# Kernel optimization log

Hardware: AMD Instinct MI355X
Metric: run time of the kernel (lower is better)

The kernel has to match this reference:

```python
import jax, jax.numpy as jnp
import numpy as np

N_EXPERTS = 8
TOPK = 2


def setup_inputs() -> dict:
    key = jax.random.key(0)
    k1, k2, k3, k4 = jax.random.split(key, 4)
    B, T, D, H, E = 2, 2048, 1024, 4096, N_EXPERTS
    s = 1.0 / np.sqrt(D)
    return {
        "x": jax.random.normal(k1, (B, T, D), dtype=jnp.float32),
        "W_gate": jax.random.normal(k2, (E, D), dtype=jnp.float32) * s,
        "W_fc": jax.random.normal(k3, (E, H, D), dtype=jnp.float32) * s,
        "W_proj": jax.random.normal(k4, (E, D, H), dtype=jnp.float32) * (1.0 / np.sqrt(H)),
    }


def reference(x, W_gate, W_fc, W_proj):
    B, T, D = x.shape
    E = W_gate.shape[0]
    N = B * T
    xf = x.reshape(N, D)

    # gating
    gate_logits = xf @ W_gate.T                       # [N, E]
    gate_probs = jax.nn.softmax(gate_logits, axis=-1)
    rw, eidx = jax.lax.top_k(gate_probs, TOPK)        # [N, K]
    rw = rw / jnp.sum(rw, axis=-1, keepdims=True)

    # exact dispatch: out[n] = sum_k rw[n,k] * MLP_{eidx[n,k]}(x[n])
    # loop over the small fixed expert count; each expert processes all tokens,
    # masked-combined by its per-token routing weight (same math as index_add dispatch).
    out = jnp.zeros_like(xf)
    for e in range(E):
        we = jnp.sum(jnp.where(eidx == e, rw, 0.0), axis=-1)     # [N]
        h = jnp.square(jax.nn.relu(xf @ W_fc[e].T))              # relu(x)^2, [N, H]
        out = out + (h @ W_proj[e].T) * we[:, None]

    # load-balance loss
    ones = jnp.ones((N * TOPK,), dtype=gate_probs.dtype)
    counts = jax.ops.segment_sum(ones, eidx.reshape(-1), num_segments=E)
    expert_freq = counts / N
    balance_loss = jnp.sum(gate_probs.mean(axis=0) * jax.lax.stop_gradient(expert_freq)) * E

    return out.reshape(B, T, D), balance_loss
```

## Files before the change

kernel.cpp:

```cpp
#include <hip/hip_runtime.h>
#include <hip/hip_bf16.h>
#include <math.h>

#define N_TOK 4096
#define D_DIM 1024
#define H_DIM 4096
#define E_NUM 8
#define NSLOT (N_TOK * 2)

typedef short bf16x8 __attribute__((ext_vector_type(8)));
typedef float f32x4 __attribute__((ext_vector_type(4)));


__device__ __forceinline__ unsigned short f2bf(float f) {
  unsigned int u = __float_as_uint(f);
  u += 0x7FFFu + ((u >> 16) & 1u);
  return (unsigned short)(u >> 16);
}

__device__ __forceinline__ void gld_lds16(const void* g, void* l) {
  __builtin_amdgcn_global_load_lds(
      (__attribute__((address_space(1))) void*)(g),
      (__attribute__((address_space(3))) void*)(l), 16, 0, 0);
}


__global__ void init_ctrl(int* p) { p[threadIdx.x] = 0; }

__global__ void cvt_f32_bf16(const float* __restrict__ src,
                             unsigned short* __restrict__ dst, int n4) {
  int i = blockIdx.x * blockDim.x + threadIdx.x;
  if (i >= n4) return;
  float4 v = ((const float4*)src)[i];
  ushort4 o;
  o.x = f2bf(v.x); o.y = f2bf(v.y); o.z = f2bf(v.z); o.w = f2bf(v.w);
  ((ushort4*)dst)[i] = o;
}

__global__ void zero_f32(float* __restrict__ p, int n4) {
  int i = blockIdx.x * blockDim.x + threadIdx.x;
  if (i < n4) ((float4*)p)[i] = make_float4(0.f, 0.f, 0.f, 0.f);
}


__global__ void gating_kernel(const float* __restrict__ x,
                              const float* __restrict__ wg,
                              float* __restrict__ probs,
                              int* __restrict__ eidx,
                              float* __restrict__ rw) {
  __shared__ float4 wg_lds[2048];
  const int t = threadIdx.x;
  const int lane = t & 63;
  const int wave = t >> 6;

#pragma unroll
  for (int j = 0; j < 8; ++j)
    wg_lds[t + 256 * j] = ((const float4*)wg)[t + 256 * j];
  __syncthreads();

#pragma unroll
  for (int j = 0; j < 4; ++j) {
    const int n = blockIdx.x * 16 + wave * 4 + j;
    const float4* xr = (const float4*)(x + (size_t)n * D_DIM);

    float acc[E_NUM];
#pragma unroll
    for (int e = 0; e < E_NUM; ++e) acc[e] = 0.f;

#pragma unroll
    for (int i = 0; i < 4; ++i) {
      float4 xv = xr[lane + 64 * i];
#pragma unroll
      for (int e = 0; e < E_NUM; ++e) {
        float4 wv = wg_lds[e * 256 + lane + 64 * i];
        acc[e] += xv.x * wv.x + xv.y * wv.y + xv.z * wv.z + xv.w * wv.w;
      }
    }
#pragma unroll
    for (int m = 1; m < 64; m <<= 1) {
#pragma unroll
      for (int e = 0; e < E_NUM; ++e) acc[e] += __shfl_xor(acc[e], m, 64);
    }

    float mx = acc[0];
#pragma unroll
    for (int e = 1; e < E_NUM; ++e) mx = fmaxf(mx, acc[e]);
    float p[E_NUM], s = 0.f;
#pragma unroll
    for (int e = 0; e < E_NUM; ++e) { p[e] = __expf(acc[e] - mx); s += p[e]; }
    float inv = 1.f / s;

    if (lane < E_NUM) probs[(size_t)n * E_NUM + lane] = p[lane] * inv;

    if (lane == 0) {
      int i1 = 0;
#pragma unroll
      for (int e = 1; e < E_NUM; ++e) if (p[e] > p[i1]) i1 = e;
      int i2 = (i1 == 0) ? 1 : 0;
#pragma unroll
      for (int e = 0; e < E_NUM; ++e)
        if (e != i1 && p[e] > p[i2]) i2 = e;
      float p1 = p[i1], p2 = p[i2];
      float wsum = 1.f / (p1 + p2);
      eidx[n] = i1 | (i2 << 8);
      rw[2 * n] = p1 * wsum;
      rw[2 * n + 1] = p2 * wsum;
    }
  }
}

__global__ void reduce_route(const float* __restrict__ probs,
                             const int* __restrict__ eidx,
                             int* __restrict__ counts,
                             int* __restrict__ offsets,
                             float* __restrict__ loss) {
  const int t = threadIdx.x;
  float4 part = make_float4(0.f, 0.f, 0.f, 0.f);
  for (int j = 0; j < 32; ++j) {
    float4 v = ((const float4*)probs)[t + 256 * j];
    part.x += v.x; part.y += v.y; part.z += v.z; part.w += v.w;
  }
  int cnt[E_NUM];
#pragma unroll
  for (int e = 0; e < E_NUM; ++e) cnt[e] = 0;
  for (int j = 0; j < 16; ++j) {
    int pk = eidx[t + 256 * j];
    int e1 = pk & 255, e2 = pk >> 8;
#pragma unroll
    for (int e = 0; e < E_NUM; ++e) cnt[e] += (e1 == e) + (e2 == e);
  }

  __shared__ float redf[256 * E_NUM];
  __shared__ int redi[256 * E_NUM];
  const int eb = (t & 1) * 4;
#pragma unroll
  for (int e = 0; e < E_NUM; ++e) { redf[t * E_NUM + e] = 0.f; redi[t * E_NUM + e] = cnt[e]; }
  redf[t * E_NUM + eb + 0] = part.x;
  redf[t * E_NUM + eb + 1] = part.y;
  redf[t * E_NUM + eb + 2] = part.z;
  redf[t * E_NUM + eb + 3] = part.w;
  __syncthreads();
  for (int s = 128; s > 0; s >>= 1) {
    if (t < s) {
#pragma unroll
      for (int e = 0; e < E_NUM; ++e) {
        redf[t * E_NUM + e] += redf[(t + s) * E_NUM + e];
        redi[t * E_NUM + e] += redi[(t + s) * E_NUM + e];
      }
    }
    __syncthreads();
  }
  if (t == 0) {
    int o = 0;
    float L = 0.f;
    for (int e = 0; e < E_NUM; ++e) {
      int c = redi[e];
      counts[e] = c;
      offsets[e] = o;
      o += c;
      L += redf[e] * (float)c;
    }
    loss[0] = L * (float)E_NUM / ((float)N_TOK * (float)N_TOK);
  }
}

__global__ void scatter_kernel(const int* __restrict__ eidx, const float* __restrict__ rw,
                               const int* __restrict__ offsets, int* __restrict__ cursor,
                               int* __restrict__ tok_id, float* __restrict__ tok_w) {
  __shared__ int lcnt[E_NUM];
  __shared__ int lbase[E_NUM];
  const int t = threadIdx.x;
  const int n = blockIdx.x * 256 + t;
  if (t < E_NUM) lcnt[t] = 0;
  __syncthreads();
  int pk = eidx[n];
  int e1 = pk & 255, e2 = pk >> 8;
  int p1 = atomicAdd(&lcnt[e1], 1);
  int p2 = atomicAdd(&lcnt[e2], 1);
  __syncthreads();
  if (t < E_NUM) lbase[t] = atomicAdd(&cursor[t], lcnt[t]);
  __syncthreads();
  int d1 = offsets[e1] + lbase[e1] + p1;
  tok_id[d1] = n; tok_w[d1] = rw[2 * n];
  int d2 = offsets[e2] + lbase[e2] + p2;
  tok_id[d2] = n; tok_w[d2] = rw[2 * n + 1];
}


__launch_bounds__(256, 2)
__global__ void gemm_fc(const unsigned short* __restrict__ xb,
                        const unsigned short* __restrict__ wfc,
                        const int* __restrict__ tok_id,
                        const int* __restrict__ counts,
                        const int* __restrict__ offsets,
                        unsigned short* __restrict__ hbuf) {
  const int e = blockIdx.z;
  const int cnt = counts[e];
  const int mtile = blockIdx.y;
  if (mtile * 128 >= cnt) return;
  const int ntile = blockIdx.x;
  const int off = offsets[e];

  __shared__ __align__(16) unsigned short As[128 * 64];
  __shared__ __align__(16) unsigned short Bs[128 * 64];

  const int t = threadIdx.x;
  const int lane = t & 63;
  const int wave = t >> 6;
  const int wm = (wave >> 1) * 64;
  const int wn = (wave & 1) * 64;
  const int srow = t >> 3;
  const int seg = (t & 7) ^ (srow & 7);

  const unsigned short* aptr[4];
  const unsigned short* bptr[4];
#pragma unroll
  for (int p = 0; p < 4; ++p) {
    int r = mtile * 128 + p * 32 + srow;
    r = (r < cnt) ? r : (cnt - 1);
    int tok = tok_id[off + r];
    aptr[p] = xb + (size_t)tok * D_DIM + seg * 8;
    int br = ntile * 128 + p * 32 + srow;
    bptr[p] = wfc + ((size_t)e * H_DIM + br) * D_DIM + seg * 8;
  }

  f32x4 acc[4][4];
#pragma unroll
  for (int i = 0; i < 4; ++i)
#pragma unroll
    for (int j = 0; j < 4; ++j) acc[i][j] = (f32x4){0.f, 0.f, 0.f, 0.f};

  const int frow_a = wm + (lane & 15);
  const int frow_b = wn + (lane & 15);
  const int q = lane >> 4;
  const int csw = lane & 7;

  for (int k0 = 0; k0 < D_DIM; k0 += 64) {
#pragma unroll
    for (int p = 0; p < 4; ++p) {
      gld_lds16(aptr[p] + k0, &As[p * 2048 + t * 8]);
      gld_lds16(bptr[p] + k0, &Bs[p * 2048 + t * 8]);
    }
    __syncthreads();
#pragma unroll
    for (int kk = 0; kk < 64; kk += 32) {
      const int ca = ((((kk >> 3) + q) ^ csw) << 3);
      bf16x8 af[4], bfr[4];
#pragma unroll
      for (int i = 0; i < 4; ++i)
        af[i] = *(const bf16x8*)&As[(frow_a + i * 16) * 64 + ca];
#pragma unroll
      for (int j = 0; j < 4; ++j)
        bfr[j] = *(const bf16x8*)&Bs[(frow_b + j * 16) * 64 + ca];
#pragma unroll
      for (int i = 0; i < 4; ++i)
#pragma unroll
        for (int j = 0; j < 4; ++j)
          acc[i][j] = __builtin_amdgcn_mfma_f32_16x16x32_bf16(af[i], bfr[j], acc[i][j], 0, 0, 0);
    }
    __syncthreads();
  }

  const int lm = (lane >> 4) * 4;
  const int ln = lane & 15;
#pragma unroll
  for (int i = 0; i < 4; ++i) {
#pragma unroll
    for (int r = 0; r < 4; ++r) {
      int m = mtile * 128 + wm + i * 16 + lm + r;
      if (m < cnt) {
        size_t rowbase = (size_t)(off + m) * H_DIM + ntile * 128 + wn;
#pragma unroll
        for (int j = 0; j < 4; ++j) {
          float v = acc[i][j][r];
          v = v > 0.f ? v * v : 0.f;
          hbuf[rowbase + j * 16 + ln] = f2bf(v);
        }
      }
    }
  }
}

__launch_bounds__(256, 2)
__global__ void gemm_proj(const unsigned short* __restrict__ hbuf,
                          const unsigned short* __restrict__ wproj,
                          const int* __restrict__ tok_id,
                          const float* __restrict__ tok_w,
                          const int* __restrict__ counts,
                          const int* __restrict__ offsets,
                          float* __restrict__ out) {
  const int e = blockIdx.z >> 1;
  const int kbase = (blockIdx.z & 1) * (H_DIM / 2);
  const int cnt = counts[e];
  const int mtile = blockIdx.y;
  if (mtile * 128 >= cnt) return;
  const int ntile = blockIdx.x;
  const int off = offsets[e];

  __shared__ __align__(16) unsigned short As[128 * 64];
  __shared__ __align__(16) unsigned short Bs[128 * 64];

  const int t = threadIdx.x;
  const int lane = t & 63;
  const int wave = t >> 6;
  const int wm = (wave >> 1) * 64;
  const int wn = (wave & 1) * 64;
  const int srow = t >> 3;
  const int seg = (t & 7) ^ (srow & 7);

  const unsigned short* aptr[4];
  const unsigned short* bptr[4];
#pragma unroll
  for (int p = 0; p < 4; ++p) {
    int r = mtile * 128 + p * 32 + srow;
    r = (r < cnt) ? r : (cnt - 1);
    aptr[p] = hbuf + (size_t)(off + r) * H_DIM + seg * 8;
    int br = ntile * 128 + p * 32 + srow;
    bptr[p] = wproj + ((size_t)e * D_DIM + br) * H_DIM + seg * 8;
  }

  f32x4 acc[4][4];
#pragma unroll
  for (int i = 0; i < 4; ++i)
#pragma unroll
    for (int j = 0; j < 4; ++j) acc[i][j] = (f32x4){0.f, 0.f, 0.f, 0.f};

  const int frow_a = wm + (lane & 15);
  const int frow_b = wn + (lane & 15);
  const int q = lane >> 4;
  const int csw = lane & 7;

  for (int k0 = kbase; k0 < kbase + H_DIM / 2; k0 += 64) {
#pragma unroll
    for (int p = 0; p < 4; ++p) {
      gld_lds16(aptr[p] + k0, &As[p * 2048 + t * 8]);
      gld_lds16(bptr[p] + k0, &Bs[p * 2048 + t * 8]);
    }
    __syncthreads();
#pragma unroll
    for (int kk = 0; kk < 64; kk += 32) {
      const int ca = ((((kk >> 3) + q) ^ csw) << 3);
      bf16x8 af[4], bfr[4];
#pragma unroll
      for (int i = 0; i < 4; ++i)
        af[i] = *(const bf16x8*)&As[(frow_a + i * 16) * 64 + ca];
#pragma unroll
      for (int j = 0; j < 4; ++j)
        bfr[j] = *(const bf16x8*)&Bs[(frow_b + j * 16) * 64 + ca];
#pragma unroll
      for (int i = 0; i < 4; ++i)
#pragma unroll
        for (int j = 0; j < 4; ++j)
          acc[i][j] = __builtin_amdgcn_mfma_f32_16x16x32_bf16(af[i], bfr[j], acc[i][j], 0, 0, 0);
    }
    __syncthreads();
  }

  const int lm = (lane >> 4) * 4;
  const int ln = lane & 15;
#pragma unroll
  for (int i = 0; i < 4; ++i) {
#pragma unroll
    for (int r = 0; r < 4; ++r) {
      int m = mtile * 128 + wm + i * 16 + lm + r;
      if (m < cnt) {
        int slot = off + m;
        float w = tok_w[slot];
        float* orow = out + (size_t)tok_id[slot] * D_DIM + ntile * 128 + wn;
#pragma unroll
        for (int j = 0; j < 4; ++j)
          atomicAdd(&orow[j * 16 + ln], acc[i][j][r] * w);
      }
    }
  }
}


extern "C" void kernel_launch(void* const* d_in, const int* in_sizes, int n_in,
                              void* d_out, int out_size, void* d_ws, size_t ws_size,
                              hipStream_t stream) {
  (void)in_sizes; (void)n_in; (void)out_size; (void)ws_size;
  const float* x = (const float*)d_in[0];
  const float* wg = (const float*)d_in[1];
  const float* wfc = (const float*)d_in[2];
  const float* wproj = (const float*)d_in[3];
  float* out = (float*)d_out;
  char* ws = (char*)d_ws;

  int* counts = (int*)(ws + 0);
  int* cursor = (int*)(ws + 64);
  int* offsets = (int*)(ws + 128);
  int* eidx = (int*)(ws + 256);
  float* rw = (float*)(ws + 16640);
  int* tok_id = (int*)(ws + 49408);
  float* tok_w = (float*)(ws + 82176);
  float* probs = (float*)(ws + 114944);
  unsigned short* xb = (unsigned short*)(ws + 246016);
  unsigned short* wfcb = (unsigned short*)(ws + 8634624);
  unsigned short* wpjb = (unsigned short*)(ws + 75743488);
  unsigned short* hbuf = (unsigned short*)(ws + 142852352);

  hipLaunchKernelGGL(init_ctrl, dim3(1), dim3(64), 0, stream, (int*)ws);
  hipLaunchKernelGGL(cvt_f32_bf16, dim3(32768), dim3(256), 0, stream, wfc, wfcb, 8388608);
  hipLaunchKernelGGL(cvt_f32_bf16, dim3(32768), dim3(256), 0, stream, wproj, wpjb, 8388608);
  hipLaunchKernelGGL(cvt_f32_bf16, dim3(4096), dim3(256), 0, stream, x, xb, 1048576);
  hipLaunchKernelGGL(zero_f32, dim3(4096), dim3(256), 0, stream, out, 1048576);
  hipLaunchKernelGGL(gating_kernel, dim3(256), dim3(256), 0, stream, x, wg, probs, eidx, rw);
  hipLaunchKernelGGL(reduce_route, dim3(1), dim3(256), 0, stream, probs, eidx, counts, offsets, out + 4194304);
  hipLaunchKernelGGL(scatter_kernel, dim3(16), dim3(256), 0, stream, eidx, rw, offsets, cursor, tok_id, tok_w);
  hipLaunchKernelGGL(gemm_fc, dim3(32, 32, 8), dim3(256), 0, stream, xb, wfcb, tok_id, counts, offsets, hbuf);
  hipLaunchKernelGGL(gemm_proj, dim3(8, 32, 16), dim3(256), 0, stream, hbuf, wpjb, tok_id, tok_w, counts, offsets, out);
}
```

Measured before the change: 562.0 us.

## Fuse conversions and routing, replace atomic scatter-add with partial buffers and combine

Merges the two weight conversion kernels into one launch and folds the x-to-bf16 conversion into the gating kernel. The scatter kernel and the cursor init become a prefix scan inside reduce_route, which also records an inverse slot map. gemm_proj now writes plain float4 partial sums per K-half into a buffer that reuses the fc-weight workspace, and a new combine kernel does the weighted gather-sum, replacing float atomics and the output zeroing. The MFMA B-fragment mapping changes so epilogues can store vectorised ushort4/float4, which alters the LDS swizzle access pattern. In exchange the code adds an extra kernel and roughly 64MB of partial-buffer traffic.

```diff
diff --git a/kernel.cpp b/kernel.cpp
--- a/kernel.cpp
+++ b/kernel.cpp
@@ -25,21 +25,21 @@
 }
 
 
-__global__ void init_ctrl(int* p) { p[threadIdx.x] = 0; }
-
-__global__ void cvt_f32_bf16(const float* __restrict__ src,
-                             unsigned short* __restrict__ dst, int n4) {
-  int i = blockIdx.x * blockDim.x + threadIdx.x;
-  if (i >= n4) return;
-  float4 v = ((const float4*)src)[i];
+__global__ void cvt_w(const float* __restrict__ wfc, const float* __restrict__ wproj,
+                      unsigned short* __restrict__ wfcb, unsigned short* __restrict__ wpjb) {
+  int i = blockIdx.x * 256 + threadIdx.x;
+  float4 v;
   ushort4 o;
-  o.x = f2bf(v.x); o.y = f2bf(v.y); o.z = f2bf(v.z); o.w = f2bf(v.w);
-  ((ushort4*)dst)[i] = o;
-}
-
-__global__ void zero_f32(float* __restrict__ p, int n4) {
-  int i = blockIdx.x * blockDim.x + threadIdx.x;
-  if (i < n4) ((float4*)p)[i] = make_float4(0.f, 0.f, 0.f, 0.f);
+  if (i < 8388608) {
+    v = ((const float4*)wfc)[i];
+    o.x = f2bf(v.x); o.y = f2bf(v.y); o.z = f2bf(v.z); o.w = f2bf(v.w);
+    ((ushort4*)wfcb)[i] = o;
+  } else {
+    int k = i - 8388608;
+    v = ((const float4*)wproj)[k];
+    o.x = f2bf(v.x); o.y = f2bf(v.y); o.z = f2bf(v.z); o.w = f2bf(v.w);
+    ((ushort4*)wpjb)[k] = o;
+  }
 }
 
 
@@ -47,7 +47,8 @@
                               const float* __restrict__ wg,
                               float* __restrict__ probs,
                               int* __restrict__ eidx,
-                              float* __restrict__ rw) {
+                              float* __restrict__ rw,
+                              unsigned short* __restrict__ xb) {
   __shared__ float4 wg_lds[2048];
   const int t = threadIdx.x;
   const int lane = t & 63;
@@ -62,6 +63,7 @@
   for (int j = 0; j < 4; ++j) {
     const int n = blockIdx.x * 16 + wave * 4 + j;
     const float4* xr = (const float4*)(x + (size_t)n * D_DIM);
+    ushort4* xw = (ushort4*)(xb + (size_t)n * D_DIM);
 
     float acc[E_NUM];
 #pragma unroll
@@ -70,6 +72,9 @@
 #pragma unroll
     for (int i = 0; i < 4; ++i) {
       float4 xv = xr[lane + 64 * i];
+      ushort4 xo;
+      xo.x = f2bf(xv.x); xo.y = f2bf(xv.y); xo.z = f2bf(xv.z); xo.w = f2bf(xv.w);
+      xw[lane + 64 * i] = xo;
 #pragma unroll
       for (int e = 0; e < E_NUM; ++e) {
         float4 wv = wg_lds[e * 256 + lane + 64 * i];
@@ -109,10 +114,14 @@
   }
 }
 
+
 __global__ void reduce_route(const float* __restrict__ probs,
                              const int* __restrict__ eidx,
                              int* __restrict__ counts,
                              int* __restrict__ offsets,
+                             int* __restrict__ tok_id,
+                             int* __restrict__ inv,
+                             const float* __restrict__ rw_unused,
                              float* __restrict__ loss) {
   const int t = threadIdx.x;
   float4 part = make_float4(0.f, 0.f, 0.f, 0.f);
@@ -123,18 +132,33 @@
   int cnt[E_NUM];
 #pragma unroll
   for (int e = 0; e < E_NUM; ++e) cnt[e] = 0;
+  int pkc[16];
   for (int j = 0; j < 16; ++j) {
     int pk = eidx[t + 256 * j];
+    pkc[j] = pk;
     int e1 = pk & 255, e2 = pk >> 8;
 #pragma unroll
     for (int e = 0; e < E_NUM; ++e) cnt[e] += (e1 == e) + (e2 == e);
   }
 
+  __shared__ int sc[256 * 9];
+#pragma unroll
+  for (int e = 0; e < E_NUM; ++e) sc[t * 9 + e] = cnt[e];
+  __syncthreads();
+  for (int s = 1; s < 256; s <<= 1) {
+    int v[E_NUM];
+#pragma unroll
+    for (int e = 0; e < E_NUM; ++e) v[e] = (t >= s) ? sc[(t - s) * 9 + e] : 0;
+    __syncthreads();
+#pragma unroll
+    for (int e = 0; e < E_NUM; ++e) sc[t * 9 + e] += v[e];
+    __syncthreads();
+  }
+
   __shared__ float redf[256 * E_NUM];
-  __shared__ int redi[256 * E_NUM];
   const int eb = (t & 1) * 4;
 #pragma unroll
-  for (int e = 0; e < E_NUM; ++e) { redf[t * E_NUM + e] = 0.f; redi[t * E_NUM + e] = cnt[e]; }
+  for (int e = 0; e < E_NUM; ++e) redf[t * E_NUM + e] = 0.f;
   redf[t * E_NUM + eb + 0] = part.x;
   redf[t * E_NUM + eb + 1] = part.y;
   redf[t * E_NUM + eb + 2] = part.z;
@@ -143,47 +167,47 @@
   for (int s = 128; s > 0; s >>= 1) {
     if (t < s) {
 #pragma unroll
-      for (int e = 0; e < E_NUM; ++e) {
+      for (int e = 0; e < E_NUM; ++e)
         redf[t * E_NUM + e] += redf[(t + s) * E_NUM + e];
-        redi[t * E_NUM + e] += redi[(t + s) * E_NUM + e];
-      }
-    }
-    __syncthreads();
-  }
+    }
+    __syncthreads();
+  }
+
+  __shared__ int offs_s[E_NUM];
   if (t == 0) {
     int o = 0;
     float L = 0.f;
     for (int e = 0; e < E_NUM; ++e) {
-      int c = redi[e];
+      int c = sc[255 * 9 + e];
       counts[e] = c;
       offsets[e] = o;
+      offs_s[e] = o;
       o += c;
       L += redf[e] * (float)c;
     }
     loss[0] = L * (float)E_NUM / ((float)N_TOK * (float)N_TOK);
   }
-}
-
-__global__ void scatter_kernel(const int* __restrict__ eidx, const float* __restrict__ rw,
-                               const int* __restrict__ offsets, int* __restrict__ cursor,
-                               int* __restrict__ tok_id, float* __restrict__ tok_w) {
-  __shared__ int lcnt[E_NUM];
-  __shared__ int lbase[E_NUM];
-  const int t = threadIdx.x;
-  const int n = blockIdx.x * 256 + t;
-  if (t < E_NUM) lcnt[t] = 0;
   __syncthreads();
-  int pk = eidx[n];
-  int e1 = pk & 255, e2 = pk >> 8;
-  int p1 = atomicAdd(&lcnt[e1], 1);
-  int p2 = atomicAdd(&lcnt[e2], 1);
-  __syncthreads();
-  if (t < E_NUM) lbase[t] = atomicAdd(&cursor[t], lcnt[t]);
-  __syncthreads();
-  int d1 = offsets[e1] + lbase[e1] + p1;
-  tok_id[d1] = n; tok_w[d1] = rw[2 * n];
-  int d2 = offsets[e2] + lbase[e2] + p2;
-  tok_id[d2] = n; tok_w[d2] = rw[2 * n + 1];
+
+  int base[E_NUM];
+#pragma unroll
+  for (int e = 0; e < E_NUM; ++e) base[e] = offs_s[e] + sc[t * 9 + e] - cnt[e];
+  for (int j = 0; j < 16; ++j) {
+    int n = t + 256 * j;
+    int pk = pkc[j];
+    int e1 = pk & 255, e2 = pk >> 8;
+    int pos1 = 0, pos2 = 0;
+#pragma unroll
+    for (int e = 0; e < E_NUM; ++e) {
+      if (e1 == e) pos1 = base[e]++;
+    }
+#pragma unroll
+    for (int e = 0; e < E_NUM; ++e) {
+      if (e2 == e) pos2 = base[e]++;
+    }
+    tok_id[pos1] = n; inv[2 * n] = pos1;
+    tok_id[pos2] = n; inv[2 * n + 1] = pos2;
+  }
 }
 
 
@@ -230,10 +254,8 @@
 #pragma unroll
     for (int j = 0; j < 4; ++j) acc[i][j] = (f32x4){0.f, 0.f, 0.f, 0.f};
 
-  const int frow_a = wm + (lane & 15);
-  const int frow_b = wn + (lane & 15);
+  const int ln = lane & 15;
   const int q = lane >> 4;
-  const int csw = lane & 7;
 
   for (int k0 = 0; k0 < D_DIM; k0 += 64) {
 #pragma unroll
@@ -244,14 +266,16 @@
     __syncthreads();
 #pragma unroll
     for (int kk = 0; kk < 64; kk += 32) {
-      const int ca = ((((kk >> 3) + q) ^ csw) << 3);
+      const int g = (kk >> 3) + q;
       bf16x8 af[4], bfr[4];
 #pragma unroll
       for (int i = 0; i < 4; ++i)
-        af[i] = *(const bf16x8*)&As[(frow_a + i * 16) * 64 + ca];
-#pragma unroll
-      for (int j = 0; j < 4; ++j)
-        bfr[j] = *(const bf16x8*)&Bs[(frow_b + j * 16) * 64 + ca];
+        af[i] = *(const bf16x8*)&As[(wm + ln + i * 16) * 64 + ((g ^ (ln & 7)) << 3)];
+#pragma unroll
+      for (int j = 0; j < 4; ++j) {
+        int rb = wn + 4 * ln + j;
+        bfr[j] = *(const bf16x8*)&Bs[rb * 64 + ((g ^ (rb & 7)) << 3)];
+      }
 #pragma unroll
       for (int i = 0; i < 4; ++i)
 #pragma unroll
@@ -261,21 +285,20 @@
     __syncthreads();
   }
 
-  const int lm = (lane >> 4) * 4;
-  const int ln = lane & 15;
 #pragma unroll
   for (int i = 0; i < 4; ++i) {
 #pragma unroll
     for (int r = 0; r < 4; ++r) {
-      int m = mtile * 128 + wm + i * 16 + lm + r;
+      int m = mtile * 128 + wm + i * 16 + q * 4 + r;
       if (m < cnt) {
-        size_t rowbase = (size_t)(off + m) * H_DIM + ntile * 128 + wn;
-#pragma unroll
-        for (int j = 0; j < 4; ++j) {
-          float v = acc[i][j][r];
-          v = v > 0.f ? v * v : 0.f;
-          hbuf[rowbase + j * 16 + ln] = f2bf(v);
-        }
+        float v0 = acc[i][0][r], v1 = acc[i][1][r], v2 = acc[i][2][r], v3 = acc[i][3][r];
+        v0 = v0 > 0.f ? v0 * v0 : 0.f;
+        v1 = v1 > 0.f ? v1 * v1 : 0.f;
+        v2 = v2 > 0.f ? v2 * v2 : 0.f;
+        v3 = v3 > 0.f ? v3 * v3 : 0.f;
+        ushort4 o;
+        o.x = f2bf(v0); o.y = f2bf(v1); o.z = f2bf(v2); o.w = f2bf(v3);
+        *(ushort4*)&hbuf[(size_t)(off + m) * H_DIM + ntile * 128 + wn + 4 * ln] = o;
       }
     }
   }
@@ -284,13 +307,12 @@
 __launch_bounds__(256, 2)
 __global__ void gemm_proj(const unsigned short* __restrict__ hbuf,
                           const unsigned short* __restrict__ wproj,
-                          const int* __restrict__ tok_id,
-                          const float* __restrict__ tok_w,
                           const int* __restrict__ counts,
                           const int* __restrict__ offsets,
-                          float* __restrict__ out) {
+                          float* __restrict__ partial) {
   const int e = blockIdx.z >> 1;
-  const int kbase = (blockIdx.z & 1) * (H_DIM / 2);
+  const int kq = blockIdx.z & 1;
+  const int kbase = kq * (H_DIM / 2);
   const int cnt = counts[e];
   const int mtile = blockIdx.y;
   if (mtile * 128 >= cnt) return;
@@ -325,10 +347,8 @@
 #pragma unroll
     for (int j = 0; j < 4; ++j) acc[i][j] = (f32x4){0.f, 0.f, 0.f, 0.f};
 
-  const int frow_a = wm + (lane & 15);
-  const int frow_b = wn + (lane & 15);
+  const int ln = lane & 15;
   const int q = lane >> 4;
-  const int csw = lane & 7;
 
   for (int k0 = kbase; k0 < kbase + H_DIM / 2; k0 += 64) {
 #pragma unroll
@@ -339,14 +359,16 @@
     __syncthreads();
 #pragma unroll
     for (int kk = 0; kk < 64; kk += 32) {
-      const int ca = ((((kk >> 3) + q) ^ csw) << 3);
+      const int g = (kk >> 3) + q;
       bf16x8 af[4], bfr[4];
 #pragma unroll
       for (int i = 0; i < 4; ++i)
-        af[i] = *(const bf16x8*)&As[(frow_a + i * 16) * 64 + ca];
-#pragma unroll
-      for (int j = 0; j < 4; ++j)
-        bfr[j] = *(const bf16x8*)&Bs[(frow_b + j * 16) * 64 + ca];
+        af[i] = *(const bf16x8*)&As[(wm + ln + i * 16) * 64 + ((g ^ (ln & 7)) << 3)];
+#pragma unroll
+      for (int j = 0; j < 4; ++j) {
+        int rb = wn + 4 * ln + j;
+        bfr[j] = *(const bf16x8*)&Bs[rb * 64 + ((g ^ (rb & 7)) << 3)];
+      }
 #pragma unroll
       for (int i = 0; i < 4; ++i)
 #pragma unroll
@@ -356,23 +378,39 @@
     __syncthreads();
   }
 
-  const int lm = (lane >> 4) * 4;
-  const int ln = lane & 15;
 #pragma unroll
   for (int i = 0; i < 4; ++i) {
 #pragma unroll
     for (int r = 0; r < 4; ++r) {
-      int m = mtile * 128 + wm + i * 16 + lm + r;
+      int m = mtile * 128 + wm + i * 16 + q * 4 + r;
       if (m < cnt) {
-        int slot = off + m;
-        float w = tok_w[slot];
-        float* orow = out + (size_t)tok_id[slot] * D_DIM + ntile * 128 + wn;
-#pragma unroll
-        for (int j = 0; j < 4; ++j)
-          atomicAdd(&orow[j * 16 + ln], acc[i][j][r] * w);
+        float4 o = make_float4(acc[i][0][r], acc[i][1][r], acc[i][2][r], acc[i][3][r]);
+        *(float4*)&partial[((size_t)(kq * NSLOT + off + m)) * D_DIM + ntile * 128 + wn + 4 * ln] = o;
       }
     }
   }
+}
+
+__global__ void combine(const float* __restrict__ partial,
+                        const int* __restrict__ inv,
+                        const float* __restrict__ rw,
+                        float* __restrict__ out) {
+  const int n = blockIdx.x;
+  const int t = threadIdx.x;
+  const int d1 = inv[2 * n], d2 = inv[2 * n + 1];
+  const float w1 = rw[2 * n], w2 = rw[2 * n + 1];
+  const float4* p0 = (const float4*)partial;
+  const float4* p1 = (const float4*)(partial + (size_t)NSLOT * D_DIM);
+  float4 a = p0[(size_t)d1 * 256 + t];
+  float4 b = p1[(size_t)d1 * 256 + t];
+  float4 c = p0[(size_t)d2 * 256 + t];
+  float4 d = p1[(size_t)d2 * 256 + t];
+  float4 o;
+  o.x = w1 * (a.x + b.x) + w2 * (c.x + d.x);
+  o.y = w1 * (a.y + b.y) + w2 * (c.y + d.y);
+  o.z = w1 * (a.z + b.z) + w2 * (c.z + d.z);
+  o.w = w1 * (a.w + b.w) + w2 * (c.w + d.w);
+  ((float4*)out)[(size_t)n * 256 + t] = o;
 }
 
 
@@ -388,26 +426,23 @@
   char* ws = (char*)d_ws;
 
   int* counts = (int*)(ws + 0);
-  int* cursor = (int*)(ws + 64);
-  int* offsets = (int*)(ws + 128);
+  int* offsets = (int*)(ws + 64);
   int* eidx = (int*)(ws + 256);
   float* rw = (float*)(ws + 16640);
   int* tok_id = (int*)(ws + 49408);
-  float* tok_w = (float*)(ws + 82176);
+  int* inv = (int*)(ws + 82176);
   float* probs = (float*)(ws + 114944);
   unsigned short* xb = (unsigned short*)(ws + 246016);
   unsigned short* wfcb = (unsigned short*)(ws + 8634624);
+  float* partial = (float*)(ws + 8634624);
   unsigned short* wpjb = (unsigned short*)(ws + 75743488);
   unsigned short* hbuf = (unsigned short*)(ws + 142852352);
 
-  hipLaunchKernelGGL(init_ctrl, dim3(1), dim3(64), 0, stream, (int*)ws);
-  hipLaunchKernelGGL(cvt_f32_bf16, dim3(32768), dim3(256), 0, stream, wfc, wfcb, 8388608);
-  hipLaunchKernelGGL(cvt_f32_bf16, dim3(32768), dim3(256), 0, stream, wproj, wpjb, 8388608);
-  hipLaunchKernelGGL(cvt_f32_bf16, dim3(4096), dim3(256), 0, stream, x, xb, 1048576);
-  hipLaunchKernelGGL(zero_f32, dim3(4096), dim3(256), 0, stream, out, 1048576);
-  hipLaunchKernelGGL(gating_kernel, dim3(256), dim3(256), 0, stream, x, wg, probs, eidx, rw);
-  hipLaunchKernelGGL(reduce_route, dim3(1), dim3(256), 0, stream, probs, eidx, counts, offsets, out + 4194304);
-  hipLaunchKernelGGL(scatter_kernel, dim3(16), dim3(256), 0, stream, eidx, rw, offsets, cursor, tok_id, tok_w);
+  hipLaunchKernelGGL(cvt_w, dim3(65536), dim3(256), 0, stream, wfc, wproj, wfcb, wpjb);
+  hipLaunchKernelGGL(gating_kernel, dim3(256), dim3(256), 0, stream, x, wg, probs, eidx, rw, xb);
+  hipLaunchKernelGGL(reduce_route, dim3(1), dim3(256), 0, stream, probs, eidx, counts, offsets,
+                     tok_id, inv, rw, out + 4194304);
   hipLaunchKernelGGL(gemm_fc, dim3(32, 32, 8), dim3(256), 0, stream, xb, wfcb, tok_id, counts, offsets, hbuf);
-  hipLaunchKernelGGL(gemm_proj, dim3(8, 32, 16), dim3(256), 0, stream, hbuf, wpjb, tok_id, tok_w, counts, offsets, out);
-}
+  hipLaunchKernelGGL(gemm_proj, dim3(8, 32, 16), dim3(256), 0, stream, hbuf, wpjb, counts, offsets, partial);
+  hipLaunchKernelGGL(combine, dim3(4096), dim3(256), 0, stream, partial, inv, rw, out);
+}
```

Measured after the change: 562.6 us. About the same (+0.1%).
